# Optimization experiments

Hardware: AMD Instinct MI355X
Metric: run time of the kernel (lower is better)

The kernel has to match this reference:

```python
import jax, jax.numpy as jnp
import numpy as np

D = 512
H = 8
DH = D // H
FF = 2 * D
EPS = 1e-5


def _layernorm(x, g, b):
    mu = jnp.mean(x, axis=-1, keepdims=True)
    var = jnp.mean(jnp.square(x - mu), axis=-1, keepdims=True)
    return (x - mu) * jax.lax.rsqrt(var + EPS) * g + b


def setup_inputs() -> dict:
    key = jax.random.key(0)
    ks = jax.random.split(key, 8)
    s = 0.02
    x = jax.random.normal(ks[0], (1, 4096, D), dtype=jnp.float32)
    w_qkv = jax.random.normal(ks[1], (D, 3 * D), dtype=jnp.float32) * s
    b_qkv = jnp.zeros((3 * D,), jnp.float32)
    w_out = jax.random.normal(ks[2], (D, D), dtype=jnp.float32) * s
    b_out = jnp.zeros((D,), jnp.float32)
    w_ff1 = jax.random.normal(ks[3], (D, FF), dtype=jnp.float32) * s
    b_ff1 = jnp.zeros((FF,), jnp.float32)
    w_ff2 = jax.random.normal(ks[4], (FF, D), dtype=jnp.float32) * s
    b_ff2 = jnp.zeros((D,), jnp.float32)
    g1 = jnp.ones((D,), jnp.float32)
    bt1 = jnp.zeros((D,), jnp.float32)
    g2 = jnp.ones((D,), jnp.float32)
    bt2 = jnp.zeros((D,), jnp.float32)
    return {"x": x, "w_qkv": w_qkv, "b_qkv": b_qkv, "w_out": w_out, "b_out": b_out,
            "w_ff1": w_ff1, "b_ff1": b_ff1, "w_ff2": w_ff2, "b_ff2": b_ff2,
            "g1": g1, "bt1": bt1, "g2": g2, "bt2": bt2}


def reference(x, w_qkv, b_qkv, w_out, b_out, w_ff1, b_ff1, w_ff2, b_ff2, g1, bt1, g2, bt2):
    B, S, _ = x.shape
    h = _layernorm(x, g1, bt1)
    qkv = h @ w_qkv + b_qkv                      # [B,S,3D]
    qkv = qkv.reshape(B, S, 3, H, DH)
    q, k, v = qkv[:, :, 0], qkv[:, :, 1], qkv[:, :, 2]   # [B,S,H,DH]
    scores = jnp.einsum('bqhd,bkhd->bhqk', q, k) / np.sqrt(DH).astype(np.float32)
    causal = jnp.tril(jnp.ones((S, S), dtype=bool))
    scores = jnp.where(causal, scores, -jnp.inf)
    attn = jax.nn.softmax(scores, axis=-1)
    out = jnp.einsum('bhqk,bkhd->bqhd', attn, v).reshape(B, S, D)
    x = x + out @ w_out + b_out
    h2 = _layernorm(x, g2, bt2)
    ff = jax.nn.gelu(h2 @ w_ff1 + b_ff1, approximate=False) @ w_ff2 + b_ff2
    return x + ff
```

## Files before the change

### kernel.cpp

```cpp
#include <hip/hip_runtime.h>
#include <math.h>

#define D 512
#define H 8
#define DH 64
#define S 4096
#define FF 1024

typedef __attribute__((ext_vector_type(8))) short bf16x8;
typedef __attribute__((ext_vector_type(4))) float f32x4;
typedef __attribute__((ext_vector_type(16))) float f32x16;

__device__ __forceinline__ unsigned short f2bf(float f) {
    union { float f; unsigned u; } c; c.f = f;
    unsigned r = (c.u + 0x7fff + ((c.u >> 16) & 1)) >> 16;
    return (unsigned short)r;
}
__device__ __forceinline__ float bf2f(unsigned short u) {
    union { unsigned u; float f; } c; c.u = ((unsigned)u) << 16;
    return c.f;
}

__device__ __forceinline__ void gl_lds16(const void* g, void* l) {
    __builtin_amdgcn_global_load_lds(
        (const __attribute__((address_space(1))) void*)g,
        (__attribute__((address_space(3))) void*)l, 16, 0, 0);
}

__global__ __launch_bounds__(256) void transpose_all(const float* __restrict__ wqkv,
                                                     const float* __restrict__ wout,
                                                     const float* __restrict__ wff1,
                                                     const float* __restrict__ wff2,
                                                     unsigned short* __restrict__ oqkv,
                                                     unsigned short* __restrict__ oout,
                                                     unsigned short* __restrict__ off1,
                                                     unsigned short* __restrict__ off2) {
    __shared__ unsigned short tile[32][33];
    int id = blockIdx.x;
    const float* src; unsigned short* dst; int K, N, lid;
    if (id < 768)       { src = wqkv; dst = oqkv; K = 512;  N = 1536; lid = id; }
    else if (id < 1024) { src = wout; dst = oout; K = 512;  N = 512;  lid = id - 768; }
    else if (id < 1536) { src = wff1; dst = off1; K = 512;  N = 1024; lid = id - 1024; }
    else                { src = wff2; dst = off2; K = 1024; N = 512;  lid = id - 1536; }
    int nb = N / 32;
    int n0 = (lid % nb) * 32, k0 = (lid / nb) * 32;
    int tx = threadIdx.x & 31, ty = threadIdx.x >> 5;
#pragma unroll
    for (int i = 0; i < 32; i += 8)
        tile[ty + i][tx] = f2bf(src[(size_t)(k0 + ty + i) * N + n0 + tx]);
    __syncthreads();
#pragma unroll
    for (int i = 0; i < 32; i += 8)
        dst[(size_t)(n0 + ty + i) * K + k0 + tx] = tile[tx][ty + i];
}

__global__ __launch_bounds__(256) void transpose_v(const unsigned short* __restrict__ qkv,
                                                   unsigned short* __restrict__ vT) {
    __shared__ unsigned short tile[32][33];
    int s0 = blockIdx.x * 32, d0 = blockIdx.y * 32;
    int tx = threadIdx.x & 31, ty = threadIdx.x >> 5;
#pragma unroll
    for (int i = 0; i < 32; i += 8)
        tile[ty + i][tx] = qkv[(size_t)(s0 + ty + i) * (3 * D) + 2 * D + d0 + tx];
    __syncthreads();
#pragma unroll
    for (int i = 0; i < 32; i += 8)
        vT[(size_t)(d0 + ty + i) * S + s0 + tx] = tile[tx][ty + i];
}

__global__ __launch_bounds__(256) void ln_kernel(const float* __restrict__ x,
                                                 const float* __restrict__ g,
                                                 const float* __restrict__ bta,
                                                 unsigned short* __restrict__ out) {
    int row = blockIdx.x, tid = threadIdx.x;
    const float* xr = x + (size_t)row * D;
    float2 v = *(const float2*)(xr + tid * 2);
    float s = v.x + v.y;
    float sq = v.x * v.x + v.y * v.y;
#pragma unroll
    for (int m = 1; m < 64; m <<= 1) { s += __shfl_xor(s, m); sq += __shfl_xor(sq, m); }
    __shared__ float red[8];
    int wave = tid >> 6, lane = tid & 63;
    if (lane == 0) { red[wave] = s; red[4 + wave] = sq; }
    __syncthreads();
    s = red[0] + red[1] + red[2] + red[3];
    sq = red[4] + red[5] + red[6] + red[7];
    float mu = s * (1.f / D);
    float var = sq * (1.f / D) - mu * mu;
    float rstd = rsqrtf(var + 1e-5f);
    int i = tid * 2;
    float2 gg = *(const float2*)(g + i);
    float2 bb = *(const float2*)(bta + i);
    out[(size_t)row * D + i]     = f2bf((v.x - mu) * rstd * gg.x + bb.x);
    out[(size_t)row * D + i + 1] = f2bf((v.y - mu) * rstd * gg.y + bb.y);
}

enum { EPI_BF16 = 0, EPI_RESID_F32 = 1, EPI_GELU_BF16 = 2 };

template <int EPI, int WMI>
__global__ __launch_bounds__(256, WMI == 4 ? 3 : 4)
void gemm2_kernel(const unsigned short* __restrict__ A,
                  const unsigned short* __restrict__ BT,
                  const float* __restrict__ bias,
                  const float* __restrict__ resid,
                  void* __restrict__ out,
                  int M, int N, int K) {
    constexpr int BM = 32 * WMI;
    constexpr int BN = 128;
    constexpr int APH = BM * 8 / 256;
    __shared__ __align__(16) unsigned short sA[BM * 64];
    __shared__ __align__(16) unsigned short sB[BN * 64];

    int tid = threadIdx.x;
    int wave = tid >> 6, lane = tid & 63;
    int quad = lane >> 4, l16 = lane & 15;
    int lx = l16 & 7;
    int wr = (wave >> 1) * (BM / 2), wc = (wave & 1) * 64;
    int m0 = blockIdx.y * BM, n0 = blockIdx.x * BN;

    f32x4 acc[WMI][4];
#pragma unroll
    for (int i = 0; i < WMI; i++)
#pragma unroll
        for (int j = 0; j < 4; j++) acc[i][j] = (f32x4){0.f, 0.f, 0.f, 0.f};

    int srow = tid >> 3;
    int spc = tid & 7;
    int scc = spc ^ (srow & 7);
    const unsigned short* Abase = A + (size_t)(m0 + srow) * K + scc * 8;
    const unsigned short* Bbase = BT + (size_t)(n0 + srow) * K + scc * 8;
    unsigned short* sAdst = sA + (tid & ~63) * 8;
    unsigned short* sBdst = sB + (tid & ~63) * 8;

    for (int k0 = 0; k0 < K; k0 += 64) {
        __syncthreads();
#pragma unroll
        for (int ph = 0; ph < APH; ph++)
            gl_lds16(Abase + (size_t)(ph * 32) * K + k0, sAdst + ph * 256 * 8);
#pragma unroll
        for (int ph = 0; ph < 4; ph++)
            gl_lds16(Bbase + (size_t)(ph * 32) * K + k0, sBdst + ph * 256 * 8);
        asm volatile("s_waitcnt vmcnt(0)" ::: "memory");
        __syncthreads();

#pragma unroll
        for (int ks = 0; ks < 2; ks++) {
            int cxs = ((ks * 4 + quad) ^ lx) * 8;
            bf16x8 af[WMI], bfr[4];
#pragma unroll
            for (int mi = 0; mi < WMI; mi++)
                af[mi] = *(const bf16x8*)(sA + (wr + mi * 16 + l16) * 64 + (cxs ^ (0)));
#pragma unroll
            for (int ni = 0; ni < 4; ni++)
                bfr[ni] = *(const bf16x8*)(sB + (wc + ni * 16 + l16) * 64 + cxs);
#pragma unroll
            for (int mi = 0; mi < WMI; mi++)
#pragma unroll
                for (int ni = 0; ni < 4; ni++)
                    acc[mi][ni] = __builtin_amdgcn_mfma_f32_16x16x32_bf16(af[mi], bfr[ni], acc[mi][ni], 0, 0, 0);
        }
    }

#pragma unroll
    for (int mi = 0; mi < WMI; mi++)
#pragma unroll
        for (int ni = 0; ni < 4; ni++) {
            int col = n0 + wc + ni * 16 + l16;
            float bs = bias[col];
#pragma unroll
            for (int r = 0; r < 4; r++) {
                int row = m0 + wr + mi * 16 + quad * 4 + r;
                float v = acc[mi][ni][r] + bs;
                size_t idx = (size_t)row * N + col;
                if constexpr (EPI == EPI_RESID_F32) {
                    ((float*)out)[idx] = v + resid[idx];
                } else if constexpr (EPI == EPI_GELU_BF16) {
                    v = 0.5f * v * (1.f + erff(v * 0.70710678118f));
                    ((unsigned short*)out)[idx] = f2bf(v);
                } else {
                    ((unsigned short*)out)[idx] = f2bf(v);
                }
            }
        }
}

#define LDF 72
#define LDO 68

__global__ __launch_bounds__(256, 4) void flash5_kernel(const unsigned short* __restrict__ qkv,
                                                        const unsigned short* __restrict__ vT,
                                                        unsigned short* __restrict__ O_part,
                                                        float* __restrict__ l_part) {
    __shared__ __align__(16) unsigned short sK[2][64 * LDF];
    __shared__ __align__(16) unsigned short sV[2][64 * LDF];

    int tid = threadIdx.x;
    int w = tid >> 6, lane = tid & 63;
    int lq = lane & 31, hb = lane >> 5;

    int h = blockIdx.x & 7;
    int u = blockIdx.x >> 3;
    int Q = 31, c = 0, acc = 0;
    for (int qq = 31; qq >= 0; --qq) {
        int n = (qq >> 2) + 1;
        if (u < acc + n) { Q = qq; c = u - acc; break; }
        acc += n;
    }
    int T = 2 * Q + 2;
    int t0c = c * 8;
    int t1c = min(t0c + 8, T);
    int q0w = Q * 128 + w * 32;
    int qrow = q0w + lq;
    int qmax = q0w + 31;

    const float CEXP = 0.18033688f;

    bf16x8 qf[4];
#pragma unroll
    for (int dc = 0; dc < 4; dc++)
        qf[dc] = *(const bf16x8*)(qkv + (size_t)qrow * (3 * D) + h * DH + dc * 16 + hb * 8);

    f32x16 oa[2];
#pragma unroll
    for (int i = 0; i < 16; i++) { oa[0][i] = 0.f; oa[1][i] = 0.f; }
    float lsum = 0.f;

    int rr = tid >> 3;
    int cc8 = (tid & 7) * 8;
    const unsigned short* kgb = qkv + (size_t)rr * (3 * D) + D + h * DH + cc8;
    const unsigned short* vgb = vT + (size_t)(h * DH + rr) * S + cc8;

    bf16x8 gk0, gk1, gv0, gv1;
    auto glb = [&](int t) {
        const unsigned short* kg = kgb + (size_t)t * 64 * (3 * D);
        gk0 = *(const bf16x8*)(kg);
        gk1 = *(const bf16x8*)(kg + (size_t)32 * (3 * D));
        const unsigned short* vg = vgb + t * 64;
        gv0 = *(const bf16x8*)(vg);
        gv1 = *(const bf16x8*)(vg + (size_t)32 * S);
    };

    glb(t0c);
    for (int t = t0c; t < t1c; ++t) {
        int buf = (t - t0c) & 1;
        unsigned short* dk = &sK[buf][rr * LDF + cc8];
        *(bf16x8*)dk = gk0;
        *(bf16x8*)(dk + 32 * LDF) = gk1;
        unsigned short* dv = &sV[buf][rr * LDF + cc8];
        *(bf16x8*)dv = gv0;
        *(bf16x8*)(dv + 32 * LDF) = gv1;
        if (t + 1 < t1c) glb(t + 1);
        __syncthreads();

        if (64 * t > qmax) continue;

        f32x16 sa[2];
#pragma unroll
        for (int i = 0; i < 16; i++) { sa[0][i] = 0.f; sa[1][i] = 0.f; }
#pragma unroll
        for (int kt = 0; kt < 2; kt++)
#pragma unroll
            for (int dc = 0; dc < 4; dc++) {
                bf16x8 kf = *(const bf16x8*)(&sK[buf][(kt * 32 + lq) * LDF + dc * 16 + hb * 8]);
                sa[kt] = __builtin_amdgcn_mfma_f32_32x32x16_bf16(kf, qf[dc], sa[kt], 0, 0, 0);
            }

        bool dmask = (64 * t + 63 > qmax);
        unsigned p2[2][8];
#pragma unroll
        for (int kt = 0; kt < 2; kt++) {
            float e[16];
#pragma unroll
            for (int r = 0; r < 16; r++) {
                float v = __builtin_amdgcn_exp2f(sa[kt][r] * CEXP);
                if (dmask) {
                    int key = 64 * t + kt * 32 + (r & 3) + 8 * (r >> 2) + 4 * hb;
                    if (key > qrow) v = 0.f;
                }
                e[r] = v;
                lsum += v;
            }
#pragma unroll
            for (int rr2 = 0; rr2 < 8; rr2++)
                p2[kt][rr2] = ((unsigned)f2bf(e[2 * rr2 + 1]) << 16) | f2bf(e[2 * rr2]);
        }

#pragma unroll
        for (int kc = 0; kc < 4; kc++) {
            int kt = kc >> 1;
            int b0i = (kc & 1) * 4;
            unsigned a0 = p2[kt][b0i + 0], a1 = p2[kt][b0i + 1];
            unsigned b0 = p2[kt][b0i + 2], b1 = p2[kt][b0i + 3];
            unsigned s0 = hb ? a0 : b0, s1 = hb ? a1 : b1;
            unsigned x0 = __shfl_xor(s0, 32), x1 = __shfl_xor(s1, 32);
            unsigned l0 = hb ? b0 : a0, l1 = hb ? b1 : a1;
            union { unsigned u[4]; bf16x8 v; } fr;
            fr.u[0] = hb ? x0 : l0;
            fr.u[1] = hb ? x1 : l1;
            fr.u[2] = hb ? l0 : x0;
            fr.u[3] = hb ? l1 : x1;
#pragma unroll
            for (int dt = 0; dt < 2; dt++) {
                bf16x8 vf = *(const bf16x8*)(&sV[buf][(dt * 32 + lq) * LDF + kc * 16 + hb * 8]);
                oa[dt] = __builtin_amdgcn_mfma_f32_32x32x16_bf16(vf, fr.v, oa[dt], 0, 0, 0);
            }
        }
    }

    lsum += __shfl_xor(lsum, 32);
    if (hb == 0)
        l_part[((size_t)c * H + h) * S + q0w + lq] = lsum;

    __syncthreads();
    unsigned short* sOw = (unsigned short*)sK + w * 32 * LDO;
#pragma unroll
    for (int kt = 0; kt < 2; kt++)
#pragma unroll
        for (int r = 0; r < 16; r++) {
            int d = kt * 32 + (r & 3) + 8 * (r >> 2) + 4 * hb;
            sOw[lq * LDO + d] = f2bf(oa[kt][r]);
        }
    asm volatile("s_waitcnt lgkmcnt(0)" ::: "memory");
    unsigned short* Op = O_part + ((size_t)c * S + q0w) * D + h * DH;
#pragma unroll
    for (int it = 0; it < 4; it++) {
        int rq = (lane >> 3) + it * 8;
        bf16x8 val = *(const bf16x8*)(sOw + rq * LDO + (lane & 7) * 8);
        *(bf16x8*)(Op + (size_t)rq * D + (lane & 7) * 8) = val;
    }
}

__global__ __launch_bounds__(256) void norm_kernel(const unsigned short* __restrict__ O_part,
                                                   const float* __restrict__ l_part,
                                                   unsigned short* __restrict__ O) {
    int idx = blockIdx.x * 256 + threadIdx.x;
    int row = idx >> 9, col = idx & 511;
    int h = col >> 6;
    int nch = ((row >> 7) >> 2) + 1;
    float o = 0.f, l = 0.f;
    for (int cc = 0; cc < nch; cc++) {
        o += bf2f(O_part[((size_t)cc * S + row) * D + col]);
        l += l_part[((size_t)cc * H + h) * S + row];
    }
    O[idx] = f2bf(o / l);
}

extern "C" void kernel_launch(void* const* d_in, const int* in_sizes, int n_in,
                              void* d_out, int out_size, void* d_ws, size_t ws_size,
                              hipStream_t stream) {
    const float* x     = (const float*)d_in[0];
    const float* w_qkv = (const float*)d_in[1];
    const float* b_qkv = (const float*)d_in[2];
    const float* w_out = (const float*)d_in[3];
    const float* b_out = (const float*)d_in[4];
    const float* w_ff1 = (const float*)d_in[5];
    const float* b_ff1 = (const float*)d_in[6];
    const float* w_ff2 = (const float*)d_in[7];
    const float* b_ff2 = (const float*)d_in[8];
    const float* g1    = (const float*)d_in[9];
    const float* bt1   = (const float*)d_in[10];
    const float* g2    = (const float*)d_in[11];
    const float* bt2   = (const float*)d_in[12];

    char* ws = (char*)d_ws;
    size_t off = 0;
    auto alloc = [&](size_t bytes) {
        void* p = ws + off;
        off += (bytes + 255) & ~(size_t)255;
        return p;
    };
    unsigned short* hbuf   = (unsigned short*)alloc((size_t)S * D * 2);
    unsigned short* qkvbuf = (unsigned short*)alloc((size_t)S * 3 * D * 2);
    unsigned short* vTbuf  = (unsigned short*)alloc((size_t)D * S * 2);
    unsigned short* Obuf   = (unsigned short*)alloc((size_t)S * D * 2);
    unsigned short* wqkvT  = (unsigned short*)alloc((size_t)3 * D * D * 2);
    unsigned short* woutT  = (unsigned short*)alloc((size_t)D * D * 2);
    unsigned short* wff1T  = (unsigned short*)alloc((size_t)FF * D * 2);
    unsigned short* wff2T  = (unsigned short*)alloc((size_t)D * FF * 2);
    unsigned short* Opart  = (unsigned short*)alloc((size_t)8 * S * D * 2);
    float*          lpart  = (float*)alloc((size_t)8 * H * S * 4);
    unsigned short* h2buf  = hbuf;
    unsigned short* ff1buf = qkvbuf;
    float*          x2buf  = (float*)Opart;

    transpose_all<<<dim3(2048), 256, 0, stream>>>(w_qkv, w_out, w_ff1, w_ff2,
                                                  wqkvT, woutT, wff1T, wff2T);

    ln_kernel<<<S, 256, 0, stream>>>(x, g1, bt1, hbuf);
    gemm2_kernel<EPI_BF16, 4><<<dim3(12, 32), 256, 0, stream>>>(
        hbuf, wqkvT, b_qkv, nullptr, qkvbuf, S, 3 * D, D);
    transpose_v<<<dim3(S / 32, D / 32), 256, 0, stream>>>(qkvbuf, vTbuf);
    flash5_kernel<<<dim3(1152), 256, 0, stream>>>(qkvbuf, vTbuf, Opart, lpart);
    norm_kernel<<<dim3(S * D / 256), 256, 0, stream>>>(Opart, lpart, Obuf);
    gemm2_kernel<EPI_RESID_F32, 2><<<dim3(4, 64), 256, 0, stream>>>(
        Obuf, woutT, b_out, x, x2buf, S, D, D);
    ln_kernel<<<S, 256, 0, stream>>>(x2buf, g2, bt2, h2buf);
    gemm2_kernel<EPI_GELU_BF16, 4><<<dim3(8, 32), 256, 0, stream>>>(
        h2buf, wff1T, b_ff1, nullptr, ff1buf, S, FF, D);
    gemm2_kernel<EPI_RESID_F32, 2><<<dim3(4, 64), 256, 0, stream>>>(
        ff1buf, wff2T, b_ff2, x2buf, (float*)d_out, S, D, FF);
}
```

Before: 205.7 us.

## Prescale Q, cheapen softmax packing, split lsum, and shrink GEMM M-tiles

```diff
diff --git a/kernel.cpp b/kernel.cpp
--- a/kernel.cpp
+++ b/kernel.cpp
@@ -19,6 +19,9 @@
 __device__ __forceinline__ float bf2f(unsigned short u) {
     union { unsigned u; float f; } c; c.u = ((unsigned)u) << 16;
     return c.f;
+}
+__device__ __forceinline__ unsigned asu(float f) {
+    union { float f; unsigned u; } c; c.f = f; return c.u;
 }
 
 __device__ __forceinline__ void gl_lds16(const void* g, void* l) {
@@ -149,7 +152,7 @@
             bf16x8 af[WMI], bfr[4];
 #pragma unroll
             for (int mi = 0; mi < WMI; mi++)
-                af[mi] = *(const bf16x8*)(sA + (wr + mi * 16 + l16) * 64 + (cxs ^ (0)));
+                af[mi] = *(const bf16x8*)(sA + (wr + mi * 16 + l16) * 64 + cxs);
 #pragma unroll
             for (int ni = 0; ni < 4; ni++)
                 bfr[ni] = *(const bf16x8*)(sB + (wc + ni * 16 + l16) * 64 + cxs);
@@ -187,7 +190,7 @@
 #define LDF 72
 #define LDO 68
 
-__global__ __launch_bounds__(256, 4) void flash5_kernel(const unsigned short* __restrict__ qkv,
+__global__ __launch_bounds__(256, 4) void flash6_kernel(const unsigned short* __restrict__ qkv,
                                                         const unsigned short* __restrict__ vT,
                                                         unsigned short* __restrict__ O_part,
                                                         float* __restrict__ l_part) {
@@ -217,13 +220,19 @@
 
     bf16x8 qf[4];
 #pragma unroll
-    for (int dc = 0; dc < 4; dc++)
-        qf[dc] = *(const bf16x8*)(qkv + (size_t)qrow * (3 * D) + h * DH + dc * 16 + hb * 8);
+    for (int dc = 0; dc < 4; dc++) {
+        bf16x8 qraw = *(const bf16x8*)(qkv + (size_t)qrow * (3 * D) + h * DH + dc * 16 + hb * 8);
+        bf16x8 qs;
+#pragma unroll
+        for (int j = 0; j < 8; j++)
+            qs[j] = (short)f2bf(bf2f((unsigned short)qraw[j]) * CEXP);
+        qf[dc] = qs;
+    }
 
     f32x16 oa[2];
 #pragma unroll
     for (int i = 0; i < 16; i++) { oa[0][i] = 0.f; oa[1][i] = 0.f; }
-    float lsum = 0.f;
+    float l4[4] = {0.f, 0.f, 0.f, 0.f};
 
     int rr = tid >> 3;
     int cc8 = (tid & 7) * 8;
@@ -267,22 +276,37 @@
 
         bool dmask = (64 * t + 63 > qmax);
         unsigned p2[2][8];
-#pragma unroll
-        for (int kt = 0; kt < 2; kt++) {
-            float e[16];
-#pragma unroll
-            for (int r = 0; r < 16; r++) {
-                float v = __builtin_amdgcn_exp2f(sa[kt][r] * CEXP);
-                if (dmask) {
+        if (!dmask) {
+#pragma unroll
+            for (int kt = 0; kt < 2; kt++) {
+                float e[16];
+#pragma unroll
+                for (int r = 0; r < 16; r++) {
+                    e[r] = __builtin_amdgcn_exp2f(sa[kt][r]);
+                    l4[r & 3] += e[r];
+                }
+#pragma unroll
+                for (int p = 0; p < 8; p++)
+                    p2[kt][p] = __builtin_amdgcn_perm(asu(e[2 * p + 1]) + 0x8000u,
+                                                      asu(e[2 * p]) + 0x8000u, 0x07060302u);
+            }
+        } else {
+#pragma unroll
+            for (int kt = 0; kt < 2; kt++) {
+                float e[16];
+#pragma unroll
+                for (int r = 0; r < 16; r++) {
+                    float v = __builtin_amdgcn_exp2f(sa[kt][r]);
                     int key = 64 * t + kt * 32 + (r & 3) + 8 * (r >> 2) + 4 * hb;
                     if (key > qrow) v = 0.f;
+                    e[r] = v;
+                    l4[r & 3] += v;
                 }
-                e[r] = v;
-                lsum += v;
+#pragma unroll
+                for (int p = 0; p < 8; p++)
+                    p2[kt][p] = __builtin_amdgcn_perm(asu(e[2 * p + 1]) + 0x8000u,
+                                                      asu(e[2 * p]) + 0x8000u, 0x07060302u);
             }
-#pragma unroll
-            for (int rr2 = 0; rr2 < 8; rr2++)
-                p2[kt][rr2] = ((unsigned)f2bf(e[2 * rr2 + 1]) << 16) | f2bf(e[2 * rr2]);
         }
 
 #pragma unroll
@@ -307,6 +331,7 @@
         }
     }
 
+    float lsum = (l4[0] + l4[1]) + (l4[2] + l4[3]);
     lsum += __shfl_xor(lsum, 32);
     if (hb == 0)
         l_part[((size_t)c * H + h) * S + q0w + lq] = lsum;
@@ -387,15 +412,15 @@
                                                   wqkvT, woutT, wff1T, wff2T);
 
     ln_kernel<<<S, 256, 0, stream>>>(x, g1, bt1, hbuf);
-    gemm2_kernel<EPI_BF16, 4><<<dim3(12, 32), 256, 0, stream>>>(
+    gemm2_kernel<EPI_BF16, 2><<<dim3(12, 64), 256, 0, stream>>>(
         hbuf, wqkvT, b_qkv, nullptr, qkvbuf, S, 3 * D, D);
     transpose_v<<<dim3(S / 32, D / 32), 256, 0, stream>>>(qkvbuf, vTbuf);
-    flash5_kernel<<<dim3(1152), 256, 0, stream>>>(qkvbuf, vTbuf, Opart, lpart);
+    flash6_kernel<<<dim3(1152), 256, 0, stream>>>(qkvbuf, vTbuf, Opart, lpart);
     norm_kernel<<<dim3(S * D / 256), 256, 0, stream>>>(Opart, lpart, Obuf);
     gemm2_kernel<EPI_RESID_F32, 2><<<dim3(4, 64), 256, 0, stream>>>(
         Obuf, woutT, b_out, x, x2buf, S, D, D);
     ln_kernel<<<S, 256, 0, stream>>>(x2buf, g2, bt2, h2buf);
-    gemm2_kernel<EPI_GELU_BF16, 4><<<dim3(8, 32), 256, 0, stream>>>(
+    gemm2_kernel<EPI_GELU_BF16, 2><<<dim3(8, 64), 256, 0, stream>>>(
         h2buf, wff1T, b_ff1, nullptr, ff1buf, S, FF, D);
     gemm2_kernel<EPI_RESID_F32, 2><<<dim3(4, 64), 256, 0, stream>>>(
         ff1buf, wff2T, b_ff2, x2buf, (float*)d_out, S, D, FF);
```

Result: no change. 205.2 us (-0.3%).
